# Kernel tuning notes

Hardware: AMD Instinct MI355X
Metric: run time of the kernel (lower is better)

Reference implementation:

```python
import jax, jax.numpy as jnp
import numpy as np

B, T, S, D, H = 16, 128, 128, 512, 100

def setup_inputs() -> dict:
    key = jax.random.key(0)
    ks = jax.random.split(key, 10)
    sc = 0.02
    return {
        "input": jax.random.normal(ks[0], (B, T, D), dtype=jnp.float32),
        "memory_bank": jax.random.normal(ks[1], (B, S, D), dtype=jnp.float32),
        "W_in": jax.random.normal(ks[2], (D, D), dtype=jnp.float32) * sc,   # linear_in, no bias
        "W1": jax.random.normal(ks[3], (H, 2 * D), dtype=jnp.float32) * sc,  # linear_1
        "b1": jnp.zeros((H,), dtype=jnp.float32),
        "W2": jax.random.normal(ks[4], (H, H), dtype=jnp.float32) * sc,      # linear_2
        "b2": jnp.zeros((H,), dtype=jnp.float32),
        "w_mean": jax.random.normal(ks[5], (H,), dtype=jnp.float32) * sc,    # mean_out
        "b_mean": jnp.zeros((1,), dtype=jnp.float32),
        "w_var": jax.random.normal(ks[6], (H,), dtype=jnp.float32) * sc,     # var_out
        "b_var": jnp.zeros((1,), dtype=jnp.float32),
        "W_out": jax.random.normal(ks[7], (D, 2 * D), dtype=jnp.float32) * sc,  # linear_out, no bias
    }


def reference(input, memory_bank, W_in, W1, b1, W2, b2, w_mean, b_mean, w_var, b_var, W_out):
    d = input.shape[-1]
    # score(): linear_in(h_t) then bmm with h_s^T -> [B,T,S]
    ht = jnp.einsum('btd,ed->bte', input, W_in)
    align = jnp.einsum('bte,bse->bts', ht, memory_bank)
    # softmax over source dim (no memory_lengths -> no mask)
    align_vectors = jax.nn.softmax(align, axis=-1)
    # get_raw_scores(): fused form of cat([h_t_expand, h_s_expand]) @ W1^T
    W1t, W1s = W1[:, :d], W1[:, d:]
    pt = jnp.einsum('btd,hd->bth', input, W1t)        # [B,T,H]
    ps = jnp.einsum('bsd,hd->bsh', memory_bank, W1s)  # [B,S,H]
    h1 = jax.nn.softplus(pt[:, :, None, :] + ps[:, None, :, :] + b1)  # [B,T,S,H]
    h2 = jax.nn.softplus(jnp.einsum('btsh,gh->btsg', h1, W2) + b2)    # [B,T,S,H]
    h_mean = jax.nn.softplus(jnp.einsum('btsg,g->bts', h2, w_mean) + b_mean[0])
    h_var = jax.nn.softplus(jnp.einsum('btsg,g->bts', h2, w_var) + b_var[0])
    # context + output projection + tanh
    c = jnp.einsum('bts,bsd->btd', align_vectors, memory_bank)
    concat_c = jnp.concatenate([c, input], axis=-1)  # [B,T,2D]
    attn_h = jnp.tanh(jnp.einsum('btf,df->btd', concat_c, W_out))
    # multi-step: transpose to [T,B,*]
    attn_h = jnp.transpose(attn_h, (1, 0, 2))
    align_vectors = jnp.transpose(align_vectors, (1, 0, 2))
    return attn_h, align_vectors, h_mean, h_var
```

## Files before the change

### kernel.cpp

```cpp
#include <hip/hip_runtime.h>
#include <hip/hip_bf16.h>
#include <math.h>

#define Bn 16
#define Tn 128
#define Sn 128
#define Dn 512
#define Hn 100
#define TT 2

typedef short short8 __attribute__((ext_vector_type(8)));
typedef float f32x4 __attribute__((ext_vector_type(4)));
typedef unsigned short ushort4v __attribute__((ext_vector_type(4)));

__device__ __forceinline__ float softplus_f(float x) {
    return fmaxf(x, 0.0f) + __logf(1.0f + __expf(-fabsf(x)));
}
__device__ __forceinline__ unsigned short f2bf(float f) {
    unsigned u = __float_as_uint(f);
    unsigned r = u + 0x7FFFu + ((u >> 16) & 1u);
    return (unsigned short)(r >> 16);
}
__device__ __forceinline__ float bf2f(unsigned short h) {
    return __uint_as_float(((unsigned)h) << 16);
}
__device__ __forceinline__ unsigned pkrn(float a, float b) {
    __hip_bfloat162 h = __float22bfloat162_rn(float2{a, b});
    return *reinterpret_cast<unsigned*>(&h);
}
struct BfPair { unsigned short h, l; };
__device__ __forceinline__ BfPair split2(float x) {
    BfPair p;
    p.h = f2bf(x);
    p.l = f2bf(x - bf2f(p.h));
    return p;
}

__global__ __launch_bounds__(256)
void conv_trans(const float* __restrict__ input, const float* __restrict__ mem,
                const float* __restrict__ W_in, const float* __restrict__ W1,
                const float* __restrict__ W_out, const float* __restrict__ W2,
                unsigned short* __restrict__ inh, unsigned short* __restrict__ inl,
                unsigned short* __restrict__ memh, unsigned short* __restrict__ meml,
                unsigned short* __restrict__ winh, unsigned short* __restrict__ winl,
                unsigned short* __restrict__ w1b, unsigned short* __restrict__ woutb,
                unsigned short* __restrict__ w2b, unsigned short* __restrict__ concatb,
                unsigned short* __restrict__ memTb)
{
    __shared__ float tile[64][65];
    const int bx = blockIdx.x;
    if (bx >= 2930) {
        const int b2x = bx - 2930;
        const int d0 = (b2x & 7) * 64, s0 = ((b2x >> 3) & 1) * 64, b = b2x >> 4;
        const int tid = threadIdx.x;
        const int r = tid >> 2, cb = (tid & 3) * 16;
        const float* src = mem + ((long)b * Sn + s0 + r) * Dn + d0 + cb;
        #pragma unroll
        for (int j = 0; j < 4; ++j) {
            float4 v = *(const float4*)&src[j * 4];
            tile[r][cb + j * 4 + 0] = v.x;
            tile[r][cb + j * 4 + 1] = v.y;
            tile[r][cb + j * 4 + 2] = v.z;
            tile[r][cb + j * 4 + 3] = v.w;
        }
        __syncthreads();
        unsigned short* dst = memTb + ((long)b * Dn + d0 + r) * Sn + s0 + cb;
        #pragma unroll
        for (int j = 0; j < 4; ++j) {
            ushort4v q;
            q.x = f2bf(tile[cb + j * 4 + 0][r]);
            q.y = f2bf(tile[cb + j * 4 + 1][r]);
            q.z = f2bf(tile[cb + j * 4 + 2][r]);
            q.w = f2bf(tile[cb + j * 4 + 3][r]);
            *(ushort4v*)&dst[j * 4] = q;
        }
        return;
    }
    long gid = (long)bx * 1024 + (long)threadIdx.x * 4;
    if (gid < 1048576) {
        float4 v = *(const float4*)&input[gid];
        BfPair a = split2(v.x), b = split2(v.y), c = split2(v.z), d = split2(v.w);
        ushort4v h = {a.h, b.h, c.h, d.h};
        ushort4v l = {a.l, b.l, c.l, d.l};
        *(ushort4v*)&inh[gid] = h;
        *(ushort4v*)&inl[gid] = l;
        long row = gid >> 9; int col = (int)(gid & 511);
        *(ushort4v*)&concatb[row * 1024 + 512 + col] = h;
    } else if (gid < 2097152) {
        long e = gid - 1048576;
        float4 v = *(const float4*)&mem[e];
        BfPair a = split2(v.x), b = split2(v.y), c = split2(v.z), d = split2(v.w);
        ushort4v h = {a.h, b.h, c.h, d.h};
        ushort4v l = {a.l, b.l, c.l, d.l};
        *(ushort4v*)&memh[e] = h;
        *(ushort4v*)&meml[e] = l;
    } else if (gid < 2359296) {
        long e = gid - 2097152;
        float4 v = *(const float4*)&W_in[e];
        BfPair a = split2(v.x), b = split2(v.y), c = split2(v.z), d = split2(v.w);
        ushort4v h = {a.h, b.h, c.h, d.h};
        ushort4v l = {a.l, b.l, c.l, d.l};
        *(ushort4v*)&winh[e] = h;
        *(ushort4v*)&winl[e] = l;
    } else if (gid < 2461696) {
        long e = gid - 2359296;
        float4 v = *(const float4*)&W1[e];
        ushort4v h = {f2bf(v.x), f2bf(v.y), f2bf(v.z), f2bf(v.w)};
        *(ushort4v*)&w1b[e] = h;
    } else if (gid < 2985984) {
        long e = gid - 2461696;
        float4 v = *(const float4*)&W_out[e];
        ushort4v h = {f2bf(v.x), f2bf(v.y), f2bf(v.z), f2bf(v.w)};
        *(ushort4v*)&woutb[e] = h;
    } else {
        long e = gid - 2985984;
        int n = (int)(e >> 7), k = (int)(e & 127);
        ushort4v h;
        #pragma unroll
        for (int j = 0; j < 4; ++j) {
            int kj = k + j;
            float val = (n < Hn && kj < Hn) ? W2[n * Hn + kj] : 0.0f;
            h[j] = f2bf(val);
        }
        *(ushort4v*)&w2b[n * 128 + k] = h;
    }
}

template<int SPLIT, int EPI, int KSPLIT, int BSEL>
__device__ __forceinline__
void gemm_body(int bx, int by, int bz_in, int upperThresh,
               const unsigned short* __restrict__ Ah, const unsigned short* __restrict__ Al,
               const unsigned short* __restrict__ Bh, const unsigned short* __restrict__ Bl,
               float* __restrict__ C, unsigned short* __restrict__ Cb,
               unsigned short* __restrict__ Cb2, const float* __restrict__ bias,
               int N, int K, int lda, int ldb, int ldc,
               long sA, long sB, long sC, long sKC,
               unsigned short* As_, unsigned short* Bs_)
{
    unsigned short* Asl = As_ + 4096;
    unsigned short* Bsl = Bs_ + 4096;

    const int tid = threadIdx.x;
    const int n0 = bx * 64;
    const long m0 = (long)by * 64;
    int bz = bz_in, kh = 0;
    if (KSPLIT) { bz = bz_in & 15; kh = bz_in >> 4; }
    Ah += (long)bz * sA;
    Bh += (long)bz * sB;
    if (SPLIT) { Al += (long)bz * sA; Bl += (long)bz * sB; }
    const bool upperB = BSEL && (by >= upperThresh);
    if (upperB) Bh += BSEL;

    const int kbeg = KSPLIT ? kh * (K / KSPLIT) : 0;
    const int kend = KSPLIT ? kbeg + (K / KSPLIT) : K;

    const int wid = tid >> 6, lane = tid & 63;
    const int lm = lane & 15, lq = lane >> 4;
    const int wm = wid & 1, wn = wid >> 1;

    const int sr = tid >> 2;
    const int sc = (tid & 3) * 2;
    const bool bok = (n0 + sr) < N;

    f32x4 acc[2][2];
    #pragma unroll
    for (int i = 0; i < 2; ++i)
        #pragma unroll
        for (int j = 0; j < 2; ++j)
            acc[i][j] = (f32x4){0.f, 0.f, 0.f, 0.f};

    for (int k0 = kbeg; k0 < kend; k0 += 64) {
        __syncthreads();
        #pragma unroll
        for (int i = 0; i < 2; ++i) {
            int c = sc + i, p = c ^ (sr & 7);
            *(short8*)&As_[sr * 64 + p * 8] =
                *(const short8*)&Ah[(m0 + sr) * lda + k0 + c * 8];
            if (SPLIT)
                *(short8*)&Asl[sr * 64 + p * 8] =
                    *(const short8*)&Al[(m0 + sr) * lda + k0 + c * 8];
        }
        #pragma unroll
        for (int i = 0; i < 2; ++i) {
            int c = sc + i, p = c ^ (sr & 7);
            short8 v = {0, 0, 0, 0, 0, 0, 0, 0};
            short8 vl = {0, 0, 0, 0, 0, 0, 0, 0};
            if (bok) {
                v = *(const short8*)&Bh[(long)(n0 + sr) * ldb + k0 + c * 8];
                if (SPLIT) vl = *(const short8*)&Bl[(long)(n0 + sr) * ldb + k0 + c * 8];
            }
            *(short8*)&Bs_[sr * 64 + p * 8] = v;
            if (SPLIT) *(short8*)&Bsl[sr * 64 + p * 8] = vl;
        }
        __syncthreads();
        #pragma unroll
        for (int kst = 0; kst < 2; ++kst) {
            short8 a[2], b[2], a2[2], b2r[2];
            const int pp = (kst * 4 + lq) ^ (lm & 7);
            #pragma unroll
            for (int mt = 0; mt < 2; ++mt) {
                int row = wm * 32 + mt * 16 + lm;
                a[mt] = *(const short8*)&As_[row * 64 + pp * 8];
                if (SPLIT) a2[mt] = *(const short8*)&Asl[row * 64 + pp * 8];
            }
            #pragma unroll
            for (int nt = 0; nt < 2; ++nt) {
                int row = wn * 32 + nt * 16 + lm;
                b[nt] = *(const short8*)&Bs_[row * 64 + pp * 8];
                if (SPLIT) b2r[nt] = *(const short8*)&Bsl[row * 64 + pp * 8];
            }
            #pragma unroll
            for (int mt = 0; mt < 2; ++mt)
                #pragma unroll
                for (int nt = 0; nt < 2; ++nt) {
                    if (SPLIT) {
                        acc[mt][nt] = __builtin_amdgcn_mfma_f32_16x16x32_bf16(
                            a2[mt], b[nt], acc[mt][nt], 0, 0, 0);
                        acc[mt][nt] = __builtin_amdgcn_mfma_f32_16x16x32_bf16(
                            a[mt], b2r[nt], acc[mt][nt], 0, 0, 0);
                    }
                    acc[mt][nt] = __builtin_amdgcn_mfma_f32_16x16x32_bf16(
                        a[mt], b[nt], acc[mt][nt], 0, 0, 0);
                }
        }
    }

    #pragma unroll
    for (int mt = 0; mt < 2; ++mt)
        #pragma unroll
        for (int nt = 0; nt < 2; ++nt)
            #pragma unroll
            for (int r = 0; r < 4; ++r) {
                long m = m0 + wm * 32 + mt * 16 + lq * 4 + r;
                int n = n0 + wn * 32 + nt * 16 + lm;
                float v = acc[mt][nt][r];
                if (EPI == 0) {
                    if (n < N)
                        C[(long)bz * sC + (long)kh * sKC + m * ldc + n] = v;
                } else if (EPI == 1) {
                    unsigned short h = f2bf(v);
                    Cb[m * ldc + n] = h;
                    Cb2[m * ldc + n] = f2bf(v - bf2f(h));
                } else if (EPI == 2) {
                    long bb = m >> 7, tt = m & 127;
                    C[tt * (Bn * Dn) + bb * Dn + n] = tanhf(v);
                } else if (EPI == 3) {
                    Cb[(long)bz * sC + m * ldc + n] = f2bf(v);
                } else {
                    float bb = (!upperB && n < Hn) ? bias[n] : 0.f;
                    C[m * ldc + n] = v + bb;
                }
            }
}

template<int SPLIT, int EPI, int KSPLIT, int BSEL>
__global__ __launch_bounds__(256)
void mfma_gemm3(const unsigned short* __restrict__ Ah, const unsigned short* __restrict__ Al,
                const unsigned short* __restrict__ Bh, const unsigned short* __restrict__ Bl,
                float* __restrict__ C, unsigned short* __restrict__ Cb,
                unsigned short* __restrict__ Cb2, const float* __restrict__ bias,
                int N, int K, int lda, int ldb, int ldc,
                long sA, long sB, long sC, long sKC)
{
    __shared__ __align__(16) unsigned short As_[(SPLIT ? 2 : 1) * 4096];
    __shared__ __align__(16) unsigned short Bs_[(SPLIT ? 2 : 1) * 4096];
    gemm_body<SPLIT, EPI, KSPLIT, BSEL>(blockIdx.x, blockIdx.y, blockIdx.z,
        (int)(gridDim.y >> 1), Ah, Al, Bh, Bl, C, Cb, Cb2, bias,
        N, K, lda, ldb, ldc, sA, sB, sC, sKC, As_, Bs_);
}

__global__ __launch_bounds__(256)
void gemm_ht_ptps(const unsigned short* __restrict__ inh, const unsigned short* __restrict__ inl,
                  const unsigned short* __restrict__ winh, const unsigned short* __restrict__ winl,
                  unsigned short* __restrict__ hth, unsigned short* __restrict__ htl,
                  const unsigned short* __restrict__ w1b, float* __restrict__ ptps,
                  const float* __restrict__ b1)
{
    __shared__ __align__(16) unsigned short As_[8192];
    __shared__ __align__(16) unsigned short Bs_[8192];
    const int id = blockIdx.x;
    if (id < 256) {
        gemm_body<1, 1, 0, 0>(id & 7, id >> 3, 0, 0,
            inh, inl, winh, winl, nullptr, hth, htl, nullptr,
            Dn, Dn, Dn, Dn, Dn, 0L, 0L, 0L, 0L, As_, Bs_);
    } else {
        const int j = id - 256;
        gemm_body<0, 4, 0, 512>(j & 1, j >> 1, 0, 32,
            inh, nullptr, w1b, nullptr, ptps, nullptr, nullptr, b1,
            Hn, Dn, Dn, 2 * Dn, 128, 0L, 0L, 0L, 0L, As_, Bs_);
    }
}

__global__ __launch_bounds__(128)
void softmax_k4(const float* __restrict__ algn, long kstride,
                float* __restrict__ av_out, unsigned short* __restrict__ avb)
{
    const int bt = blockIdx.x;
    const int b = bt >> 7, t = bt & 127;
    const int s = threadIdx.x;
    const long o = (long)bt * Sn + s;
    float v = algn[o] + algn[o + kstride] + algn[o + 2 * kstride] + algn[o + 3 * kstride];

    float m = v;
    #pragma unroll
    for (int off = 32; off > 0; off >>= 1) m = fmaxf(m, __shfl_xor(m, off));
    __shared__ float red[2];
    if ((s & 63) == 0) red[s >> 6] = m;
    __syncthreads();
    m = fmaxf(red[0], red[1]);

    float e = __expf(v - m);
    float sum = e;
    #pragma unroll
    for (int off = 32; off > 0; off >>= 1) sum += __shfl_xor(sum, off);
    __shared__ float red2[2];
    if ((s & 63) == 0) red2[s >> 6] = sum;
    __syncthreads();
    float inv = 1.0f / (red2[0] + red2[1]);

    float av = e * inv;
    av_out[(long)t * (Bn * Sn) + b * Sn + s] = av;
    avb[o] = f2bf(av);
}

__global__ __launch_bounds__(256)
void mlp_mfma4(const float* __restrict__ ptps,
               const unsigned short* __restrict__ w2b,
               const float* __restrict__ b2,
               const float* __restrict__ w_mean, const float* __restrict__ b_mean,
               const float* __restrict__ w_var, const float* __restrict__ b_var,
               float* __restrict__ mean_out, float* __restrict__ var_out)
{
    __shared__ __align__(16) unsigned short h1s[64 * 128];
    __shared__ __align__(16) unsigned short w2s[112 * 128];
    __shared__ float ptl[TT][140];
    __shared__ float b2p[112], wmp[112], wvp[112];

    const int tg = blockIdx.x;
    const int b  = blockIdx.y >> 1;
    const int s0 = (blockIdx.y & 1) * 64;
    const int tid = threadIdx.x;

    #pragma unroll
    for (int i0 = 0; i0 < 7; ++i0) {
        int i = tid + i0 * 256;
        int r_ = i >> 4, c_ = i & 15;
        *(short8*)&w2s[r_ * 128 + (c_ ^ (r_ & 7)) * 8] = *(const short8*)&w2b[i * 8];
    }
    {
        int t = tid >> 7, c = tid & 127;
        ptl[t][c + 4 * (c >> 5)] =
            ptps[((long)b * Tn + tg * TT + t) * 128 + c];
    }
    if (tid < 112) {
        b2p[tid] = (tid < Hn) ? b2[tid] : 0.f;
        wmp[tid] = (tid < Hn) ? w_mean[tid] : 0.f;
        wvp[tid] = (tid < Hn) ? w_var[tid] : 0.f;
    }

    const int r = tid >> 2, cb = tid & 3;
    float psreg[4][8];
    {
        const float* psrow = ptps + (long)(2048 + b * Sn + s0 + r) * 128;
        #pragma unroll
        for (int i = 0; i < 4; ++i) {
            int col = (cb + 4 * i) * 8;
            *(float4*)&psreg[i][0] = *(const float4*)&psrow[col];
            *(float4*)&psreg[i][4] = *(const float4*)&psrow[col + 4];
        }
    }
    __syncthreads();

    const int wid = tid >> 6, lane = tid & 63;
    const int lm = lane & 15, lq = lane >> 4;
    const float bm = b_mean[0], bv = b_var[0];

    for (int t = 0; t < TT; ++t) {
        #pragma unroll
        for (int i = 0; i < 4; ++i) {
            const int c = cb + 4 * i;
            const int col = c * 8;
            const int base = col + 4 * (col >> 5);
            float4 pa = *(const float4*)&ptl[t][base];
            float4 pb = *(const float4*)&ptl[t][base + 4];
            float x0 = softplus_f(psreg[i][0] + pa.x);
            float x1 = softplus_f(psreg[i][1] + pa.y);
            float x2 = softplus_f(psreg[i][2] + pa.z);
            float x3 = softplus_f(psreg[i][3] + pa.w);
            float x4 = softplus_f(psreg[i][4] + pb.x);
            float x5 = softplus_f(psreg[i][5] + pb.y);
            float x6 = softplus_f(psreg[i][6] + pb.z);
            float x7 = softplus_f(psreg[i][7] + pb.w);
            uint4 u;
            u.x = pkrn(x0, x1); u.y = pkrn(x2, x3);
            u.z = pkrn(x4, x5); u.w = pkrn(x6, x7);
            *(uint4*)&h1s[r * 128 + (c ^ (r & 7)) * 8] = u;
        }
        __syncthreads();

        f32x4 acc[7];
        #pragma unroll
        for (int j = 0; j < 7; ++j) acc[j] = (f32x4){0.f, 0.f, 0.f, 0.f};
        #pragma unroll
        for (int ks = 0; ks < 4; ++ks) {
            const int p = (ks * 4 + lq) ^ (lm & 7);
            short8 a = *(const short8*)&h1s[(wid * 16 + lm) * 128 + p * 8];
            #pragma unroll
            for (int nt = 0; nt < 7; ++nt) {
                short8 bf = *(const short8*)&w2s[(nt * 16 + lm) * 128 + p * 8];
                acc[nt] = __builtin_amdgcn_mfma_f32_16x16x32_bf16(a, bf, acc[nt], 0, 0, 0);
            }
        }

        float sM[4] = {}, sV[4] = {};
        #pragma unroll
        for (int nt = 0; nt < 7; ++nt) {
            int g = nt * 16 + lm;
            float bg = b2p[g], wm_ = wmp[g], wv_ = wvp[g];
            #pragma unroll
            for (int rr = 0; rr < 4; ++rr) {
                float h2 = softplus_f(acc[nt][rr] + bg);
                sM[rr] = fmaf(h2, wm_, sM[rr]);
                sV[rr] = fmaf(h2, wv_, sV[rr]);
            }
        }
        #pragma unroll
        for (int off = 1; off < 16; off <<= 1)
            #pragma unroll
            for (int rr = 0; rr < 4; ++rr) {
                sM[rr] += __shfl_xor(sM[rr], off);
                sV[rr] += __shfl_xor(sV[rr], off);
            }
        if (lm == 0) {
            const long base = ((long)b * Tn + tg * TT + t) * Sn + s0;
            #pragma unroll
            for (int rr = 0; rr < 4; ++rr) {
                int row = wid * 16 + lq * 4 + rr;
                mean_out[base + row] = softplus_f(sM[rr] + bm);
                var_out[base + row]  = softplus_f(sV[rr] + bv);
            }
        }
        __syncthreads();
    }
}

extern "C" void kernel_launch(void* const* d_in, const int* in_sizes, int n_in,
                              void* d_out, int out_size, void* d_ws, size_t ws_size,
                              hipStream_t stream)
{
    (void)in_sizes; (void)n_in; (void)out_size; (void)ws_size;

    const float* input  = (const float*)d_in[0];
    const float* mem    = (const float*)d_in[1];
    const float* W_in   = (const float*)d_in[2];
    const float* W1     = (const float*)d_in[3];
    const float* b1     = (const float*)d_in[4];
    const float* W2     = (const float*)d_in[5];
    const float* b2     = (const float*)d_in[6];
    const float* w_mean = (const float*)d_in[7];
    const float* b_mean = (const float*)d_in[8];
    const float* w_var  = (const float*)d_in[9];
    const float* b_var  = (const float*)d_in[10];
    const float* W_out  = (const float*)d_in[11];

    float* out      = (float*)d_out;
    float* attn_out = out;
    float* av_out   = out + (long)Tn * Bn * Dn;
    float* mean_out = av_out + (long)Tn * Bn * Sn;
    float* var_out  = mean_out + (long)Bn * Tn * Sn;

    char* p = (char*)d_ws;
    unsigned short* inh   = (unsigned short*)p; p += 2097152;
    unsigned short* memh  = (unsigned short*)p; p += 2097152;
    unsigned short* inl   = (unsigned short*)p; p += 2097152;
    unsigned short* meml  = (unsigned short*)p; p += 2097152;
    unsigned short* winh  = (unsigned short*)p; p += 524288;
    unsigned short* winl  = (unsigned short*)p; p += 524288;
    unsigned short* w1b   = (unsigned short*)p; p += 204800;
    unsigned short* woutb = (unsigned short*)p; p += 1048576;
    unsigned short* w2b   = (unsigned short*)p; p += 28672;
    unsigned short* memTb = (unsigned short*)p; p += 2097152;
    unsigned short* hth   = (unsigned short*)p; p += 2097152;
    unsigned short* htl   = (unsigned short*)p; p += 2097152;
    float* ptps           = (float*)p;          p += 2097152;
    float* algn           = (float*)p;          p += 4194304;
    unsigned short* avb   = (unsigned short*)p; p += 524288;
    unsigned short* concatb = (unsigned short*)p; p += 4194304;

    const long kstride = (long)Bn * Tn * Sn;

    conv_trans<<<dim3(2930 + 256), 256, 0, stream>>>(
        input, mem, W_in, W1, W_out, W2,
        inh, inl, memh, meml, winh, winl, w1b, woutb, w2b, concatb, memTb);

    gemm_ht_ptps<<<dim3(384), 256, 0, stream>>>(
        inh, inl, winh, winl, hth, htl, w1b, ptps, b1);

    mfma_gemm3<1, 0, 4, 0><<<dim3(2, 2, 64), 256, 0, stream>>>(
        hth, htl, memh, meml, algn, nullptr, nullptr, nullptr,
        Sn, Dn, Dn, Dn, Sn, (long)Tn * Dn, (long)Sn * Dn,
        (long)Tn * Sn, kstride);

    softmax_k4<<<dim3(Bn * Tn), 128, 0, stream>>>(algn, kstride, av_out, avb);

    mfma_gemm3<0, 3, 0, 0><<<dim3(8, 2, 16), 256, 0, stream>>>(
        avb, nullptr, memTb, nullptr, nullptr, concatb, nullptr, nullptr,
        Dn, Sn, Sn, Sn, 2 * Dn, (long)Tn * Sn, (long)Dn * Sn,
        (long)Tn * 2 * Dn, 0L);

    mfma_gemm3<0, 2, 0, 0><<<dim3(8, 32), 256, 0, stream>>>(
        concatb, nullptr, woutb, nullptr, attn_out, nullptr, nullptr, nullptr,
        Dn, 2 * Dn, 2 * Dn, 2 * Dn, Dn, 0L, 0L, 0L, 0L);

    mlp_mfma4<<<dim3(Tn / TT, Bn * 2), 256, 0, stream>>>(
        ptps, w2b, b2, w_mean, b_mean, w_var, b_var, mean_out, var_out);
}
```

Before: 173.7 us.

## Co-schedule align GEMM with MLP and fuse softmax into context GEMM

The align GEMM and the softplus MLP now run in one launch, with blocks split by index: 256 blocks do the split-K align GEMM and the remaining 1024 blocks do the MLP with TT raised to 4. The MLP keeps h1 in registers as MFMA B operands instead of staging it through shared memory, which removes a syncthreads per step. Softmax is fused into the context GEMM, so the bf16 probability buffer and two launches go away. The cost is that softmax is recomputed by each of the 8 N-tile blocks, and the MLP blocks share the GPU with the GEMM blocks.

```diff
diff --git a/kernel.cpp b/kernel.cpp
--- a/kernel.cpp
+++ b/kernel.cpp
@@ -7,7 +7,7 @@
 #define Sn 128
 #define Dn 512
 #define Hn 100
-#define TT 2
+#define TT 4
 
 typedef short short8 __attribute__((ext_vector_type(8)));
 typedef float f32x4 __attribute__((ext_vector_type(4)));
@@ -291,55 +291,40 @@
     }
 }
 
-__global__ __launch_bounds__(128)
-void softmax_k4(const float* __restrict__ algn, long kstride,
-                float* __restrict__ av_out, unsigned short* __restrict__ avb)
-{
-    const int bt = blockIdx.x;
-    const int b = bt >> 7, t = bt & 127;
-    const int s = threadIdx.x;
-    const long o = (long)bt * Sn + s;
-    float v = algn[o] + algn[o + kstride] + algn[o + 2 * kstride] + algn[o + 3 * kstride];
-
-    float m = v;
-    #pragma unroll
-    for (int off = 32; off > 0; off >>= 1) m = fmaxf(m, __shfl_xor(m, off));
-    __shared__ float red[2];
-    if ((s & 63) == 0) red[s >> 6] = m;
-    __syncthreads();
-    m = fmaxf(red[0], red[1]);
-
-    float e = __expf(v - m);
-    float sum = e;
-    #pragma unroll
-    for (int off = 32; off > 0; off >>= 1) sum += __shfl_xor(sum, off);
-    __shared__ float red2[2];
-    if ((s & 63) == 0) red2[s >> 6] = sum;
-    __syncthreads();
-    float inv = 1.0f / (red2[0] + red2[1]);
-
-    float av = e * inv;
-    av_out[(long)t * (Bn * Sn) + b * Sn + s] = av;
-    avb[o] = f2bf(av);
-}
-
 __global__ __launch_bounds__(256)
-void mlp_mfma4(const float* __restrict__ ptps,
+void align_mlp(const unsigned short* __restrict__ hth, const unsigned short* __restrict__ htl,
+               const unsigned short* __restrict__ memh, const unsigned short* __restrict__ meml,
+               float* __restrict__ algn, long kstride,
+               const float* __restrict__ ptps,
                const unsigned short* __restrict__ w2b,
                const float* __restrict__ b2,
                const float* __restrict__ w_mean, const float* __restrict__ b_mean,
                const float* __restrict__ w_var, const float* __restrict__ b_var,
                float* __restrict__ mean_out, float* __restrict__ var_out)
 {
-    __shared__ __align__(16) unsigned short h1s[64 * 128];
-    __shared__ __align__(16) unsigned short w2s[112 * 128];
-    __shared__ float ptl[TT][140];
-    __shared__ float b2p[112], wmp[112], wvp[112];
-
-    const int tg = blockIdx.x;
-    const int b  = blockIdx.y >> 1;
-    const int s0 = (blockIdx.y & 1) * 64;
+    __shared__ __align__(16) char smem[32768];
+    const int id = blockIdx.x;
     const int tid = threadIdx.x;
+
+    if (id < 256) {
+        unsigned short* As_ = (unsigned short*)smem;
+        unsigned short* Bs_ = (unsigned short*)(smem + 16384);
+        gemm_body<1, 0, 4, 0>(id & 1, (id >> 1) & 1, id >> 2, 0,
+            hth, htl, memh, meml, algn, nullptr, nullptr, nullptr,
+            Sn, Dn, Dn, Dn, Sn, (long)Tn * Dn, (long)Sn * Dn,
+            (long)Tn * Sn, kstride, As_, Bs_);
+        return;
+    }
+
+    unsigned short* w2s = (unsigned short*)smem;
+    float (*ptl)[132]   = (float(*)[132])(smem + 28672);
+    float* wpk          = (float*)(smem + 30784);
+    float* b2l          = (float*)(smem + 31680);
+
+    const int mid = id - 256;
+    const int tg = mid & 31;
+    const int b  = (mid >> 5) & 15;
+    const int s0 = (mid >> 9) * 64;
 
     #pragma unroll
     for (int i0 = 0; i0 < 7; ++i0) {
@@ -347,101 +332,186 @@
         int r_ = i >> 4, c_ = i & 15;
         *(short8*)&w2s[r_ * 128 + (c_ ^ (r_ & 7)) * 8] = *(const short8*)&w2b[i * 8];
     }
-    {
-        int t = tid >> 7, c = tid & 127;
-        ptl[t][c + 4 * (c >> 5)] =
-            ptps[((long)b * Tn + tg * TT + t) * 128 + c];
-    }
-    if (tid < 112) {
-        b2p[tid] = (tid < Hn) ? b2[tid] : 0.f;
-        wmp[tid] = (tid < Hn) ? w_mean[tid] : 0.f;
-        wvp[tid] = (tid < Hn) ? w_var[tid] : 0.f;
-    }
-
-    const int r = tid >> 2, cb = tid & 3;
+    #pragma unroll
+    for (int j = 0; j < 2; ++j) {
+        int i = tid + j * 256;
+        int tt = i >> 7, c = i & 127;
+        ptl[tt][c] = ptps[((long)b * Tn + tg * TT + tt) * 128 + c];
+    }
+    if (tid < 224) {
+        int g = tid >> 1;
+        wpk[tid] = (g < Hn) ? ((tid & 1) ? w_var[g] : w_mean[g]) : 0.f;
+    }
+    if (tid < 112) b2l[tid] = (tid < Hn) ? b2[tid] : 0.f;
+
+    const int wid = tid >> 6, lane = tid & 63;
+    const int lm = lane & 15, lq = lane >> 4;
+    const int s = s0 + wid * 16 + lm;
+
     float psreg[4][8];
     {
-        const float* psrow = ptps + (long)(2048 + b * Sn + s0 + r) * 128;
-        #pragma unroll
-        for (int i = 0; i < 4; ++i) {
-            int col = (cb + 4 * i) * 8;
-            *(float4*)&psreg[i][0] = *(const float4*)&psrow[col];
-            *(float4*)&psreg[i][4] = *(const float4*)&psrow[col + 4];
-        }
+        const float* psrow = ptps + (long)(2048 + b * Sn + s) * 128;
+        #pragma unroll
+        for (int ks = 0; ks < 4; ++ks) {
+            *(float4*)&psreg[ks][0] = *(const float4*)&psrow[ks * 32 + lq * 8];
+            *(float4*)&psreg[ks][4] = *(const float4*)&psrow[ks * 32 + lq * 8 + 4];
+        }
+    }
+    const float bm = b_mean[0], bv = b_var[0];
+    __syncthreads();
+
+    for (int t = 0; t < TT; ++t) {
+        short8 hf[4];
+        #pragma unroll
+        for (int ks = 0; ks < 4; ++ks) {
+            float4 pa = *(const float4*)&ptl[t][ks * 32 + lq * 8];
+            float4 pb = *(const float4*)&ptl[t][ks * 32 + lq * 8 + 4];
+            float x0 = softplus_f(psreg[ks][0] + pa.x);
+            float x1 = softplus_f(psreg[ks][1] + pa.y);
+            float x2 = softplus_f(psreg[ks][2] + pa.z);
+            float x3 = softplus_f(psreg[ks][3] + pa.w);
+            float x4 = softplus_f(psreg[ks][4] + pb.x);
+            float x5 = softplus_f(psreg[ks][5] + pb.y);
+            float x6 = softplus_f(psreg[ks][6] + pb.z);
+            float x7 = softplus_f(psreg[ks][7] + pb.w);
+            union { uint4 u4; short8 s8; } cv;
+            cv.u4.x = pkrn(x0, x1); cv.u4.y = pkrn(x2, x3);
+            cv.u4.z = pkrn(x4, x5); cv.u4.w = pkrn(x6, x7);
+            hf[ks] = cv.s8;
+        }
+        f32x4 acc[7];
+        #pragma unroll
+        for (int j = 0; j < 7; ++j) acc[j] = (f32x4){0.f, 0.f, 0.f, 0.f};
+        #pragma unroll
+        for (int ks = 0; ks < 4; ++ks) {
+            const int p = (ks * 4 + lq) ^ (lm & 7);
+            #pragma unroll
+            for (int mt = 0; mt < 7; ++mt) {
+                short8 w = *(const short8*)&w2s[(mt * 16 + lm) * 128 + p * 8];
+                acc[mt] = __builtin_amdgcn_mfma_f32_16x16x32_bf16(w, hf[ks], acc[mt], 0, 0, 0);
+            }
+        }
+        float sM = 0.f, sV = 0.f;
+        #pragma unroll
+        for (int mt = 0; mt < 7; ++mt) {
+            const int g0 = mt * 16 + lq * 4;
+            float4 bg = *(const float4*)&b2l[g0];
+            float4 wa = *(const float4*)&wpk[g0 * 2];
+            float4 wb = *(const float4*)&wpk[g0 * 2 + 4];
+            float h2;
+            h2 = softplus_f(acc[mt][0] + bg.x); sM = fmaf(h2, wa.x, sM); sV = fmaf(h2, wa.y, sV);
+            h2 = softplus_f(acc[mt][1] + bg.y); sM = fmaf(h2, wa.z, sM); sV = fmaf(h2, wa.w, sV);
+            h2 = softplus_f(acc[mt][2] + bg.z); sM = fmaf(h2, wb.x, sM); sV = fmaf(h2, wb.y, sV);
+            h2 = softplus_f(acc[mt][3] + bg.w); sM = fmaf(h2, wb.z, sM); sV = fmaf(h2, wb.w, sV);
+        }
+        sM += __shfl_xor(sM, 16); sM += __shfl_xor(sM, 32);
+        sV += __shfl_xor(sV, 16); sV += __shfl_xor(sV, 32);
+        if (lq == 0) {
+            const long base = ((long)b * Tn + tg * TT + t) * Sn + s;
+            mean_out[base] = softplus_f(sM + bm);
+            var_out[base]  = softplus_f(sV + bv);
+        }
+    }
+}
+
+__global__ __launch_bounds__(256)
+void softmax_c(const float* __restrict__ algn, long kstride,
+               const unsigned short* __restrict__ memTb,
+               float* __restrict__ av_out, unsigned short* __restrict__ concatb)
+{
+    __shared__ __align__(16) unsigned short avs[64 * 128];
+    __shared__ __align__(16) unsigned short Bs[64 * 128];
+
+    const int ntb = blockIdx.x, mtb = blockIdx.y, b = blockIdx.z;
+    const int tid = threadIdx.x;
+    const int r = tid >> 2, q = tid & 3;
+
+    float v[32];
+    {
+        const float* arow = algn + ((long)b * Tn + mtb * 64 + r) * Sn + q * 32;
+        #pragma unroll
+        for (int j = 0; j < 8; ++j) {
+            float4 a0 = *(const float4*)&arow[j * 4];
+            float4 a1 = *(const float4*)&arow[j * 4 + kstride];
+            float4 a2 = *(const float4*)&arow[j * 4 + 2 * kstride];
+            float4 a3 = *(const float4*)&arow[j * 4 + 3 * kstride];
+            v[j * 4 + 0] = a0.x + a1.x + a2.x + a3.x;
+            v[j * 4 + 1] = a0.y + a1.y + a2.y + a3.y;
+            v[j * 4 + 2] = a0.z + a1.z + a2.z + a3.z;
+            v[j * 4 + 3] = a0.w + a1.w + a2.w + a3.w;
+        }
+    }
+    float mx = v[0];
+    #pragma unroll
+    for (int i = 1; i < 32; ++i) mx = fmaxf(mx, v[i]);
+    mx = fmaxf(mx, __shfl_xor(mx, 1));
+    mx = fmaxf(mx, __shfl_xor(mx, 2));
+    float sum = 0.f;
+    #pragma unroll
+    for (int i = 0; i < 32; ++i) { v[i] = __expf(v[i] - mx); sum += v[i]; }
+    sum += __shfl_xor(sum, 1);
+    sum += __shfl_xor(sum, 2);
+    const float inv = 1.0f / sum;
+
+    if (ntb == 0) {
+        float* dst = av_out + (long)(mtb * 64 + r) * (Bn * Sn) + b * Sn + q * 32;
+        #pragma unroll
+        for (int j = 0; j < 8; ++j) {
+            float4 o = {v[j*4]*inv, v[j*4+1]*inv, v[j*4+2]*inv, v[j*4+3]*inv};
+            *(float4*)&dst[j * 4] = o;
+        }
+    }
+    #pragma unroll
+    for (int i = 0; i < 4; ++i) {
+        int c = q * 4 + i;
+        uint4 u;
+        u.x = pkrn(v[i*8+0]*inv, v[i*8+1]*inv);
+        u.y = pkrn(v[i*8+2]*inv, v[i*8+3]*inv);
+        u.z = pkrn(v[i*8+4]*inv, v[i*8+5]*inv);
+        u.w = pkrn(v[i*8+6]*inv, v[i*8+7]*inv);
+        *(uint4*)&avs[r * 128 + (c ^ (r & 7)) * 8] = u;
+    }
+    #pragma unroll
+    for (int j = 0; j < 4; ++j) {
+        int idx = tid * 4 + j;
+        int rB = idx >> 4, cB = idx & 15;
+        *(short8*)&Bs[rB * 128 + (cB ^ (rB & 7)) * 8] =
+            *(const short8*)&memTb[((long)b * Dn + ntb * 64 + rB) * Sn + cB * 8];
     }
     __syncthreads();
 
     const int wid = tid >> 6, lane = tid & 63;
     const int lm = lane & 15, lq = lane >> 4;
-    const float bm = b_mean[0], bv = b_var[0];
-
-    for (int t = 0; t < TT; ++t) {
-        #pragma unroll
-        for (int i = 0; i < 4; ++i) {
-            const int c = cb + 4 * i;
-            const int col = c * 8;
-            const int base = col + 4 * (col >> 5);
-            float4 pa = *(const float4*)&ptl[t][base];
-            float4 pb = *(const float4*)&ptl[t][base + 4];
-            float x0 = softplus_f(psreg[i][0] + pa.x);
-            float x1 = softplus_f(psreg[i][1] + pa.y);
-            float x2 = softplus_f(psreg[i][2] + pa.z);
-            float x3 = softplus_f(psreg[i][3] + pa.w);
-            float x4 = softplus_f(psreg[i][4] + pb.x);
-            float x5 = softplus_f(psreg[i][5] + pb.y);
-            float x6 = softplus_f(psreg[i][6] + pb.z);
-            float x7 = softplus_f(psreg[i][7] + pb.w);
-            uint4 u;
-            u.x = pkrn(x0, x1); u.y = pkrn(x2, x3);
-            u.z = pkrn(x4, x5); u.w = pkrn(x6, x7);
-            *(uint4*)&h1s[r * 128 + (c ^ (r & 7)) * 8] = u;
-        }
-        __syncthreads();
-
-        f32x4 acc[7];
-        #pragma unroll
-        for (int j = 0; j < 7; ++j) acc[j] = (f32x4){0.f, 0.f, 0.f, 0.f};
-        #pragma unroll
-        for (int ks = 0; ks < 4; ++ks) {
-            const int p = (ks * 4 + lq) ^ (lm & 7);
-            short8 a = *(const short8*)&h1s[(wid * 16 + lm) * 128 + p * 8];
-            #pragma unroll
-            for (int nt = 0; nt < 7; ++nt) {
-                short8 bf = *(const short8*)&w2s[(nt * 16 + lm) * 128 + p * 8];
-                acc[nt] = __builtin_amdgcn_mfma_f32_16x16x32_bf16(a, bf, acc[nt], 0, 0, 0);
-            }
-        }
-
-        float sM[4] = {}, sV[4] = {};
-        #pragma unroll
-        for (int nt = 0; nt < 7; ++nt) {
-            int g = nt * 16 + lm;
-            float bg = b2p[g], wm_ = wmp[g], wv_ = wvp[g];
+    const int wm = wid & 1, wn = wid >> 1;
+
+    f32x4 acc[2][2];
+    #pragma unroll
+    for (int i = 0; i < 2; ++i)
+        #pragma unroll
+        for (int j = 0; j < 2; ++j) acc[i][j] = (f32x4){0.f, 0.f, 0.f, 0.f};
+
+    #pragma unroll
+    for (int kk = 0; kk < 4; ++kk) {
+        const int p = (kk * 4 + lq) ^ (lm & 7);
+        short8 a0 = *(const short8*)&avs[(wm * 32 + lm) * 128 + p * 8];
+        short8 a1 = *(const short8*)&avs[(wm * 32 + 16 + lm) * 128 + p * 8];
+        short8 b0 = *(const short8*)&Bs[(wn * 32 + lm) * 128 + p * 8];
+        short8 b1 = *(const short8*)&Bs[(wn * 32 + 16 + lm) * 128 + p * 8];
+        acc[0][0] = __builtin_amdgcn_mfma_f32_16x16x32_bf16(a0, b0, acc[0][0], 0, 0, 0);
+        acc[0][1] = __builtin_amdgcn_mfma_f32_16x16x32_bf16(a0, b1, acc[0][1], 0, 0, 0);
+        acc[1][0] = __builtin_amdgcn_mfma_f32_16x16x32_bf16(a1, b0, acc[1][0], 0, 0, 0);
+        acc[1][1] = __builtin_amdgcn_mfma_f32_16x16x32_bf16(a1, b1, acc[1][1], 0, 0, 0);
+    }
+    #pragma unroll
+    for (int mt = 0; mt < 2; ++mt)
+        #pragma unroll
+        for (int nt = 0; nt < 2; ++nt)
             #pragma unroll
             for (int rr = 0; rr < 4; ++rr) {
-                float h2 = softplus_f(acc[nt][rr] + bg);
-                sM[rr] = fmaf(h2, wm_, sM[rr]);
-                sV[rr] = fmaf(h2, wv_, sV[rr]);
+                long mrow = (long)b * Tn + mtb * 64 + wm * 32 + mt * 16 + lq * 4 + rr;
+                int n = ntb * 64 + wn * 32 + nt * 16 + lm;
+                concatb[mrow * 1024 + n] = f2bf(acc[mt][nt][rr]);
             }
-        }
-        #pragma unroll
-        for (int off = 1; off < 16; off <<= 1)
-            #pragma unroll
-            for (int rr = 0; rr < 4; ++rr) {
-                sM[rr] += __shfl_xor(sM[rr], off);
-                sV[rr] += __shfl_xor(sV[rr], off);
-            }
-        if (lm == 0) {
-            const long base = ((long)b * Tn + tg * TT + t) * Sn + s0;
-            #pragma unroll
-            for (int rr = 0; rr < 4; ++rr) {
-                int row = wid * 16 + lq * 4 + rr;
-                mean_out[base + row] = softplus_f(sM[rr] + bm);
-                var_out[base + row]  = softplus_f(sV[rr] + bv);
-            }
-        }
-        __syncthreads();
-    }
 }
 
 extern "C" void kernel_launch(void* const* d_in, const int* in_sizes, int n_in,
@@ -484,7 +554,6 @@
     unsigned short* htl   = (unsigned short*)p; p += 2097152;
     float* ptps           = (float*)p;          p += 2097152;
     float* algn           = (float*)p;          p += 4194304;
-    unsigned short* avb   = (unsigned short*)p; p += 524288;
     unsigned short* concatb = (unsigned short*)p; p += 4194304;
 
     const long kstride = (long)Bn * Tn * Sn;
@@ -496,22 +565,14 @@
     gemm_ht_ptps<<<dim3(384), 256, 0, stream>>>(
         inh, inl, winh, winl, hth, htl, w1b, ptps, b1);
 
-    mfma_gemm3<1, 0, 4, 0><<<dim3(2, 2, 64), 256, 0, stream>>>(
-        hth, htl, memh, meml, algn, nullptr, nullptr, nullptr,
-        Sn, Dn, Dn, Dn, Sn, (long)Tn * Dn, (long)Sn * Dn,
-        (long)Tn * Sn, kstride);
-
-    softmax_k4<<<dim3(Bn * Tn), 128, 0, stream>>>(algn, kstride, av_out, avb);
-
-    mfma_gemm3<0, 3, 0, 0><<<dim3(8, 2, 16), 256, 0, stream>>>(
-        avb, nullptr, memTb, nullptr, nullptr, concatb, nullptr, nullptr,
-        Dn, Sn, Sn, Sn, 2 * Dn, (long)Tn * Sn, (long)Dn * Sn,
-        (long)Tn * 2 * Dn, 0L);
+    align_mlp<<<dim3(1280), 256, 0, stream>>>(
+        hth, htl, memh, meml, algn, kstride,
+        ptps, w2b, b2, w_mean, b_mean, w_var, b_var, mean_out, var_out);
+
+    softmax_c<<<dim3(8, 2, 16), 256, 0, stream>>>(
+        algn, kstride, memTb, av_out, concatb);
 
     mfma_gemm3<0, 2, 0, 0><<<dim3(8, 32), 256, 0, stream>>>(
         concatb, nullptr, woutb, nullptr, attn_out, nullptr, nullptr, nullptr,
         Dn, 2 * Dn, 2 * Dn, 2 * Dn, Dn, 0L, 0L, 0L, 0L);
-
-    mlp_mfma4<<<dim3(Tn / TT, Bn * 2), 256, 0, stream>>>(
-        ptps, w2b, b2, w_mean, b_mean, w_var, b_var, mean_out, var_out);
-}
+}
```

After: 187.2 us. 7.8% more time.
